# Kernel optimization log

Measured on AMD Instinct MI355X. Metric: run time of the kernel, lower is better.

Reference implementation:

```python
import jax, jax.numpy as jnp
import numpy as np

C = 512
NUM_HEADS = 8
GROUPS = 32
EPS_GN = 1e-5
EPS_ATTN = 1e-6


def setup_inputs() -> dict:
    key = jax.random.key(0)
    ks = jax.random.split(key, 7)
    B, H, W = 8, 64, 64
    x = jax.random.normal(ks[0], (B, C, H, W), dtype=jnp.float32)
    # GroupNorm affine (torch default: weight=1, bias=0)
    norm_gamma = jnp.ones((C,), dtype=jnp.float32)
    norm_beta = jnp.zeros((C,), dtype=jnp.float32)
    # 1x1 conv weights stored as (out, in); torch Conv2d kaiming-ish scale
    qkv_w = jax.random.normal(ks[1], (3 * C, C), dtype=jnp.float32) * (1.0 / np.sqrt(C))
    qkv_b = jax.random.normal(ks[2], (3 * C,), dtype=jnp.float32) * 0.01
    proj_w = jax.random.normal(ks[3], (C, C), dtype=jnp.float32) * (1.0 / np.sqrt(C))
    proj_b = jax.random.normal(ks[4], (C,), dtype=jnp.float32) * 0.01
    return {"x": x, "norm_gamma": norm_gamma, "norm_beta": norm_beta,
            "qkv_w": qkv_w, "qkv_b": qkv_b, "proj_w": proj_w, "proj_b": proj_b}


def _group_norm(x, gamma, beta):
    B, Cc, H, W = x.shape
    xg = x.reshape(B, GROUPS, Cc // GROUPS, H, W)
    mean = xg.mean(axis=(2, 3, 4), keepdims=True)
    var = xg.var(axis=(2, 3, 4), keepdims=True)
    xn = (xg - mean) * jax.lax.rsqrt(var + EPS_GN)
    xn = xn.reshape(B, Cc, H, W)
    return xn * gamma[None, :, None, None] + beta[None, :, None, None]


def reference(x, norm_gamma, norm_beta, qkv_w, qkv_b, proj_w, proj_b):
    B, Cc, H, W = x.shape
    h, d = NUM_HEADS, Cc // NUM_HEADS
    N = H * W
    x_norm = _group_norm(x, norm_gamma, norm_beta)
    # 1x1 conv == channel GEMM
    qkv = jnp.einsum('bchw,oc->bohw', x_norm, qkv_w) + qkv_b[None, :, None, None]
    q, k, v = jnp.split(qkv, 3, axis=1)
    # (B, C, H, W) -> (B, h, N, d)
    def to_heads(t):
        return t.reshape(B, h, d, N).transpose(0, 1, 3, 2)
    q, k, v = to_heads(q), to_heads(k), to_heads(v)
    # phi(x) = elu(x) + 1
    q = jax.nn.elu(q) + 1.0
    k = jax.nn.elu(k) + 1.0
    kv = jnp.einsum('bhnd,bhne->bhde', k, v)          # (B,h,d,d)
    out = jnp.einsum('bhnd,bhde->bhne', q, kv)        # (B,h,N,d)
    denom = jnp.einsum('bhnd,bhd->bhn', q, k.sum(axis=2))
    out = out / (denom[..., None] + EPS_ATTN)
    # (B,h,N,d) -> (B,C,H,W)
    attn = out.transpose(0, 1, 3, 2).reshape(B, Cc, H, W)
    proj = jnp.einsum('bchw,oc->bohw', attn, proj_w) + proj_b[None, :, None, None]
    # dropout is identity at inference
    return x + proj
```

## Files before the change

### kernel.cpp

```cpp
#include <hip/hip_runtime.h>
#include <math.h>

#define BATCH   8
#define CCH     512
#define NHEADS  8
#define HD      64
#define NGROUPS 32
#define CPG     16
#define NSP     4096
#define O1      1536

typedef __attribute__((ext_vector_type(8))) short          short8;
typedef __attribute__((ext_vector_type(8))) unsigned short ushort8;
typedef __attribute__((ext_vector_type(4))) unsigned short ushort4v;
typedef __attribute__((ext_vector_type(4))) float          float4v;

#define GLOAD_LDS16(g, s) __builtin_amdgcn_global_load_lds(                   \
    (const __attribute__((address_space(1))) void*)(g),                       \
    (__attribute__((address_space(3))) void*)(s), 16, 0, 0)

__device__ __forceinline__ float phi_act(float v) {
    return v > 0.f ? v + 1.f : __expf(v);
}
__device__ __forceinline__ unsigned short f2bf(float f) {
    union { float f; unsigned int u; } c; c.f = f;
    unsigned int u = c.u;
    u += 0x7fffu + ((u >> 16) & 1u);
    return (unsigned short)(u >> 16);
}
__device__ __forceinline__ float bf2f(unsigned short s) {
    union { unsigned int u; float f; } c; c.u = ((unsigned int)s) << 16;
    return c.f;
}


__global__ __launch_bounds__(256) void gn_stats(const float* __restrict__ x,
                                                const float* __restrict__ gamma,
                                                const float* __restrict__ beta,
                                                float* __restrict__ ss) {
    const int bg = blockIdx.x;
    const int t  = threadIdx.x;
    const float* base = x + (size_t)bg * (CPG * NSP);
    float s = 0.f, s2 = 0.f;
    #pragma unroll 4
    for (int i = 0; i < 64; ++i) {
        float4 v = *(const float4*)(base + (i * 256 + t) * 4);
        s  += v.x + v.y + v.z + v.w;
        s2 += v.x * v.x + v.y * v.y + v.z * v.z + v.w * v.w;
    }
    __shared__ float r1[256], r2[256];
    r1[t] = s; r2[t] = s2;
    __syncthreads();
    for (int off = 128; off > 0; off >>= 1) {
        if (t < off) { r1[t] += r1[t + off]; r2[t] += r2[t + off]; }
        __syncthreads();
    }
    if (t < CPG) {
        const float inv = 1.f / 65536.f;
        float mean = r1[0] * inv;
        float var  = r2[0] * inv - mean * mean;
        float rstd = rsqrtf(var + 1e-5f);
        int b = bg / NGROUPS, g = bg % NGROUPS;
        int c = g * CPG + t;
        float sc = gamma[c] * rstd;
        float sh = beta[c] - mean * sc;
        ss[(b * CCH + c) * 2]     = sc;
        ss[(b * CCH + c) * 2 + 1] = sh;
    }
}

__global__ __launch_bounds__(256) void conv_w(const float* __restrict__ qw,
                                              const float* __restrict__ pw,
                                              unsigned short* __restrict__ qwb,
                                              unsigned short* __restrict__ pwb,
                                              float* __restrict__ ksum) {
    int i = (blockIdx.x * 256 + threadIdx.x) * 4;
    if (i < O1 * CCH) {
        float4 v = *(const float4*)(qw + i);
        unsigned short o[4] = {f2bf(v.x), f2bf(v.y), f2bf(v.z), f2bf(v.w)};
        *(uint2*)(qwb + i) = *(uint2*)o;
    } else {
        int j = i - O1 * CCH;
        float4 v = *(const float4*)(pw + j);
        unsigned short o[4] = {f2bf(v.x), f2bf(v.y), f2bf(v.z), f2bf(v.w)};
        *(uint2*)(pwb + j) = *(uint2*)o;
    }
    if (blockIdx.x == 0) {
        float4 z = {0.f, 0.f, 0.f, 0.f};
        #pragma unroll
        for (int l = 0; l < 4; ++l)
            *(float4*)(ksum + (l * 256 + threadIdx.x) * 4) = z;
    }
}

__global__ __launch_bounds__(256) void xnT_kernel(const float* __restrict__ x,
                                                  const float* __restrict__ ss,
                                                  unsigned short* __restrict__ xnT) {
    const int n0 = blockIdx.x * 64, c0 = blockIdx.y * 64, b = blockIdx.z;
    const int t = threadIdx.x;
    __shared__ float tile[64][65];
    const float* xb  = x + ((size_t)b * CCH + c0) * NSP + n0;
    const float* ssb = ss + b * CCH * 2;

    const int lr = t / 16, lc = (t % 16) * 4;
    #pragma unroll
    for (int j = 0; j < 4; ++j) {
        int cr = j * 16 + lr;
        float4 v = *(const float4*)(xb + (size_t)cr * NSP + lc);
        float sc = ssb[(c0 + cr) * 2], sh = ssb[(c0 + cr) * 2 + 1];
        tile[cr][lc + 0] = v.x * sc + sh;
        tile[cr][lc + 1] = v.y * sc + sh;
        tile[cr][lc + 2] = v.z * sc + sh;
        tile[cr][lc + 3] = v.w * sc + sh;
    }
    __syncthreads();
    #pragma unroll
    for (int j = 0; j < 2; ++j) {
        int wd = j * 256 + t;
        int n  = wd >> 3;
        int cb = (wd & 7) * 8;
        ushort8 o;
        #pragma unroll
        for (int i = 0; i < 8; ++i) o[i] = f2bf(tile[cb + i][n]);
        *(ushort8*)(xnT + ((size_t)b * NSP + n0 + n) * CCH + c0 + cb) = o;
    }
}

__global__ __launch_bounds__(256) void gemm_q(const unsigned short* __restrict__ A,
                                              const unsigned short* __restrict__ Bt,
                                              const float* __restrict__ bias,
                                              unsigned short* __restrict__ qT) {
    const int n0 = blockIdx.x * 128;
    const int o0 = blockIdx.y * 128;
    const int b  = blockIdx.z;
    const int t  = threadIdx.x;
    const int wv = t >> 6, ln = t & 63;
    const int quad = ln >> 4, lm = ln & 15;
    const int wo = (wv >> 1) * 64, wn = (wv & 1) * 64;

    __shared__ __align__(16) unsigned short As[128 * 64];
    __shared__ __align__(16) unsigned short Bs[128 * 64];

    float4v acc[4][4];
    #pragma unroll
    for (int i = 0; i < 4; ++i)
        #pragma unroll
        for (int j = 0; j < 4; ++j) acc[i][j] = {0.f, 0.f, 0.f, 0.f};

    const unsigned short* aBase = A + (size_t)o0 * CCH;
    const unsigned short* bBase = Bt + ((size_t)b * NSP + n0) * CCH;

    const int srow8 = ln >> 3;
    const int scs   = ((ln & 7) ^ srow8) * 8;
    const int lmp   = (lm & 7);

    for (int k0 = 0; k0 < CCH; k0 += 64) {
        __syncthreads();
        #pragma unroll
        for (int i = 0; i < 4; ++i) {
            int slab = wv + i * 4;
            GLOAD_LDS16(aBase + (size_t)(slab * 8 + srow8) * CCH + k0 + scs,
                        As + slab * 512);
            GLOAD_LDS16(bBase + (size_t)(slab * 8 + srow8) * CCH + k0 + scs,
                        Bs + slab * 512);
        }
        __syncthreads();
        #pragma unroll
        for (int kk = 0; kk < 2; ++kk) {
            const int sc8 = ((kk * 4 + quad) ^ lmp) * 8;
            short8 fw[4], fx[4];
            #pragma unroll
            for (int i = 0; i < 4; ++i)
                fw[i] = *(const short8*)(As + (wo + i * 16 + lm) * 64 + sc8);
            #pragma unroll
            for (int j = 0; j < 4; ++j)
                fx[j] = *(const short8*)(Bs + (wn + j * 16 + lm) * 64 + sc8);
            #pragma unroll
            for (int i = 0; i < 4; ++i)
                #pragma unroll
                for (int j = 0; j < 4; ++j)
                    acc[i][j] = __builtin_amdgcn_mfma_f32_16x16x32_bf16(
                        fw[i], fx[j], acc[i][j], 0, 0, 0);
        }
    }

    #pragma unroll
    for (int i = 0; i < 4; ++i) {
        int ob = o0 + wo + i * 16 + quad * 4;
        float4 b4 = *(const float4*)(bias + ob);
        float bs[4] = {b4.x, b4.y, b4.z, b4.w};
        #pragma unroll
        for (int j = 0; j < 4; ++j) {
            int n = n0 + wn + j * 16 + lm;
            ushort4v pk;
            #pragma unroll
            for (int r = 0; r < 4; ++r)
                pk[r] = f2bf(phi_act(acc[i][j][r] + bs[r]));
            *(ushort4v*)(qT + ((size_t)b * NSP + n) * CCH + ob) = pk;
        }
    }
}

__global__ __launch_bounds__(256) void gemm_kv(const unsigned short* __restrict__ A,
                                               const unsigned short* __restrict__ Bt,
                                               const float* __restrict__ bias,
                                               unsigned short* __restrict__ kb,
                                               unsigned short* __restrict__ vb,
                                               float* __restrict__ ksum) {
    const int n0 = blockIdx.x * 128;
    const int o0 = 512 + blockIdx.y * 128;
    const int b  = blockIdx.z;
    const int t  = threadIdx.x;
    const int wv = t >> 6, ln = t & 63;
    const int quad = ln >> 4, lm = ln & 15;
    const int wo = (wv >> 1) * 64, wn = (wv & 1) * 64;

    __shared__ __align__(16) unsigned short As[128 * 64];
    __shared__ __align__(16) unsigned short Bs[128 * 64];

    float4v acc[4][4];
    #pragma unroll
    for (int i = 0; i < 4; ++i)
        #pragma unroll
        for (int j = 0; j < 4; ++j) acc[i][j] = {0.f, 0.f, 0.f, 0.f};

    const unsigned short* aBase = A + (size_t)o0 * CCH;
    const unsigned short* bBase = Bt + ((size_t)b * NSP + n0) * CCH;

    const int srow8 = ln >> 3;
    const int scs   = ((ln & 7) ^ srow8) * 8;
    const int lmp   = (lm & 7);

    for (int k0 = 0; k0 < CCH; k0 += 64) {
        __syncthreads();
        #pragma unroll
        for (int i = 0; i < 4; ++i) {
            int slab = wv + i * 4;
            GLOAD_LDS16(aBase + (size_t)(slab * 8 + srow8) * CCH + k0 + scs,
                        As + slab * 512);
            GLOAD_LDS16(bBase + (size_t)(slab * 8 + srow8) * CCH + k0 + scs,
                        Bs + slab * 512);
        }
        __syncthreads();
        #pragma unroll
        for (int kk = 0; kk < 2; ++kk) {
            const int sc8 = ((kk * 4 + quad) ^ lmp) * 8;
            short8 fw[4], fx[4];
            #pragma unroll
            for (int i = 0; i < 4; ++i)
                fw[i] = *(const short8*)(As + (wo + i * 16 + lm) * 64 + sc8);
            #pragma unroll
            for (int j = 0; j < 4; ++j)
                fx[j] = *(const short8*)(Bs + (wn + j * 16 + lm) * 64 + sc8);
            #pragma unroll
            for (int i = 0; i < 4; ++i)
                #pragma unroll
                for (int j = 0; j < 4; ++j)
                    acc[i][j] = __builtin_amdgcn_mfma_f32_16x16x32_bf16(
                        fx[j], fw[i], acc[i][j], 0, 0, 0);
        }
    }

    const bool isk = (o0 < 1024);
    unsigned short* dst = isk ? kb : vb;
    const int cb0 = o0 - (isk ? 512 : 1024);
    #pragma unroll
    for (int i = 0; i < 4; ++i) {
        int o = o0 + wo + i * 16 + lm;
        int c = cb0 + wo + i * 16 + lm;
        float bs = bias[o];
        float ksp = 0.f;
        #pragma unroll
        for (int j = 0; j < 4; ++j) {
            int n = n0 + wn + j * 16 + quad * 4;
            ushort4v pk;
            #pragma unroll
            for (int r = 0; r < 4; ++r) {
                float v = acc[i][j][r] + bs;
                if (isk) { v = phi_act(v); ksp += v; }
                pk[r] = f2bf(v);
            }
            *(ushort4v*)(dst + ((size_t)b * CCH + c) * NSP + n) = pk;
        }
        if (isk) {
            ksp += __shfl_xor(ksp, 16);
            ksp += __shfl_xor(ksp, 32);
            if (quad == 0) atomicAdd(ksum + b * CCH + c, ksp);
        }
    }
}

__global__ __launch_bounds__(256) void kv_mfma(const unsigned short* __restrict__ kb,
                                               const unsigned short* __restrict__ vb,
                                               float* __restrict__ kvp) {
    const int chunk = blockIdx.x, bh = blockIdx.y;
    const int b = bh >> 3, h = bh & 7;
    const int t = threadIdx.x;
    const int wv = t >> 6, ln = t & 63;
    const int quad = ln >> 4, lm = ln & 15;
    const int wd = (wv >> 1) * 32, we = (wv & 1) * 32;

    __shared__ __align__(16) unsigned short kt[2 * 64 * 32];
    __shared__ __align__(16) unsigned short vt[2 * 64 * 32];

    float4v acc[2][2];
    #pragma unroll
    for (int i = 0; i < 2; ++i)
        #pragma unroll
        for (int j = 0; j < 2; ++j) acc[i][j] = {0.f, 0.f, 0.f, 0.f};

    const unsigned short* kbase = kb + ((size_t)b * CCH + h * 64) * NSP + chunk * 1024;
    const unsigned short* vbase = vb + ((size_t)b * CCH + h * 64) * NSP + chunk * 1024;
    const int srow = ln >> 2;
    const int scs  = ((ln & 3) ^ ((ln >> 3) & 3)) * 8;
    const int sc8  = (quad ^ ((lm >> 1) & 3)) * 8;

    for (int it = 0; it < 16; ++it) {
        int noff = it * 64;
        __syncthreads();
        GLOAD_LDS16(kbase + (size_t)(wv * 16 + srow) * NSP + noff + scs,      kt + wv * 512);
        GLOAD_LDS16(kbase + (size_t)(wv * 16 + srow) * NSP + noff + 32 + scs, kt + 2048 + wv * 512);
        GLOAD_LDS16(vbase + (size_t)(wv * 16 + srow) * NSP + noff + scs,      vt + wv * 512);
        GLOAD_LDS16(vbase + (size_t)(wv * 16 + srow) * NSP + noff + 32 + scs, vt + 2048 + wv * 512);
        __syncthreads();
        #pragma unroll
        for (int kk = 0; kk < 2; ++kk) {
            short8 a0 = *(const short8*)(kt + kk * 2048 + (wd + lm) * 32 + sc8);
            short8 a1 = *(const short8*)(kt + kk * 2048 + (wd + 16 + lm) * 32 + sc8);
            short8 b0 = *(const short8*)(vt + kk * 2048 + (we + lm) * 32 + sc8);
            short8 b1 = *(const short8*)(vt + kk * 2048 + (we + 16 + lm) * 32 + sc8);
            acc[0][0] = __builtin_amdgcn_mfma_f32_16x16x32_bf16(a0, b0, acc[0][0], 0, 0, 0);
            acc[0][1] = __builtin_amdgcn_mfma_f32_16x16x32_bf16(a0, b1, acc[0][1], 0, 0, 0);
            acc[1][0] = __builtin_amdgcn_mfma_f32_16x16x32_bf16(a1, b0, acc[1][0], 0, 0, 0);
            acc[1][1] = __builtin_amdgcn_mfma_f32_16x16x32_bf16(a1, b1, acc[1][1], 0, 0, 0);
        }
    }
    #pragma unroll
    for (int i = 0; i < 2; ++i)
        #pragma unroll
        for (int j = 0; j < 2; ++j) {
            int e = we + j * 16 + lm;
            int d = wd + i * 16 + quad * 4;
            float4 r = {acc[i][j][0], acc[i][j][1], acc[i][j][2], acc[i][j][3]};
            *(float4*)(kvp + ((size_t)(chunk * 64 + bh) * 64 + e) * 64 + d) = r;
        }
}

__global__ __launch_bounds__(256) void kv_reduce(const float* __restrict__ kvp,
                                                 unsigned short* __restrict__ kvTb) {
    int idx4 = (blockIdx.x * 256 + threadIdx.x) * 4;
    float4 s = {0.f, 0.f, 0.f, 0.f};
    #pragma unroll
    for (int p = 0; p < 4; ++p) {
        float4 v = *(const float4*)(kvp + (size_t)p * (64 * 64 * 64) + idx4);
        s.x += v.x; s.y += v.y; s.z += v.z; s.w += v.w;
    }
    ushort4v o = {f2bf(s.x), f2bf(s.y), f2bf(s.z), f2bf(s.w)};
    *(ushort4v*)(kvTb + idx4) = o;
}

__global__ __launch_bounds__(256) void attn_mfma(const unsigned short* __restrict__ qT,
                                                 const unsigned short* __restrict__ kvTb,
                                                 const float* __restrict__ ksum,
                                                 unsigned short* __restrict__ attnT) {
    const int n0 = blockIdx.x * 256;
    const int bh = blockIdx.y;
    const int b = bh >> 3, h = bh & 7;
    const int t = threadIdx.x;
    const int wv = t >> 6, ln = t & 63;
    const int quad = ln >> 4, lm = ln & 15;
    const int nb = n0 + wv * 64;

    __shared__ __align__(16) unsigned short kvs[64 * 72];
    __shared__ float kss[64];

    #pragma unroll
    for (int l = 0; l < 2; ++l) {
        int ch = l * 256 + t;
        int e = ch >> 3, c8 = ch & 7;
        *(ushort8*)(kvs + e * 72 + c8 * 8) =
            *(const ushort8*)(kvTb + (size_t)bh * 4096 + ch * 8);
    }
    if (t < 64) kss[t] = ksum[b * CCH + h * 64 + t];
    __syncthreads();

    short8 bq[4][2];
    #pragma unroll
    for (int j = 0; j < 4; ++j)
        #pragma unroll
        for (int kk = 0; kk < 2; ++kk) {
            int n = nb + j * 16 + lm;
            bq[j][kk] = *(const short8*)(qT + ((size_t)b * NSP + n) * CCH +
                                         h * 64 + kk * 32 + quad * 8);
        }
    short8 ak[4][2];
    #pragma unroll
    for (int i = 0; i < 4; ++i)
        #pragma unroll
        for (int kk = 0; kk < 2; ++kk)
            ak[i][kk] = *(const short8*)(kvs + (i * 16 + lm) * 72 + kk * 32 + quad * 8);

    float4v acc[4][4];
    #pragma unroll
    for (int i = 0; i < 4; ++i)
        #pragma unroll
        for (int j = 0; j < 4; ++j) acc[i][j] = {0.f, 0.f, 0.f, 0.f};
    #pragma unroll
    for (int kk = 0; kk < 2; ++kk)
        #pragma unroll
        for (int i = 0; i < 4; ++i)
            #pragma unroll
            for (int j = 0; j < 4; ++j)
                acc[i][j] = __builtin_amdgcn_mfma_f32_16x16x32_bf16(
                    ak[i][kk], bq[j][kk], acc[i][j], 0, 0, 0);

    float rden[4];
    #pragma unroll
    for (int j = 0; j < 4; ++j) {
        float dp = 0.f;
        #pragma unroll
        for (int kk = 0; kk < 2; ++kk)
            #pragma unroll
            for (int l = 0; l < 8; ++l)
                dp += bf2f((unsigned short)bq[j][kk][l]) * kss[kk * 32 + quad * 8 + l];
        dp += __shfl_xor(dp, 16);
        dp += __shfl_xor(dp, 32);
        rden[j] = 1.f / (dp + 1e-6f);
    }

    #pragma unroll
    for (int i = 0; i < 4; ++i) {
        int e = i * 16 + quad * 4;
        #pragma unroll
        for (int j = 0; j < 4; ++j) {
            int n = nb + j * 16 + lm;
            ushort4v pk;
            #pragma unroll
            for (int r = 0; r < 4; ++r)
                pk[r] = f2bf(acc[i][j][r] * rden[j]);
            *(ushort4v*)(attnT + ((size_t)b * NSP + n) * CCH + h * 64 + e) = pk;
        }
    }
}

__global__ __launch_bounds__(256) void gemm_proj(const unsigned short* __restrict__ A,
                                                 const unsigned short* __restrict__ Bt,
                                                 const float* __restrict__ bias,
                                                 const float* __restrict__ resid,
                                                 float* __restrict__ outF) {
    const int n0 = blockIdx.x * 128;
    const int o0 = blockIdx.y * 128;
    const int b  = blockIdx.z;
    const int t  = threadIdx.x;
    const int wv = t >> 6, ln = t & 63;
    const int quad = ln >> 4, lm = ln & 15;
    const int wo = (wv >> 1) * 64, wn = (wv & 1) * 64;

    __shared__ __align__(16) unsigned short As[128 * 64];
    __shared__ __align__(16) unsigned short Bs[128 * 64];

    float4v acc[4][4];
    #pragma unroll
    for (int i = 0; i < 4; ++i)
        #pragma unroll
        for (int j = 0; j < 4; ++j) acc[i][j] = {0.f, 0.f, 0.f, 0.f};

    const unsigned short* aBase = A + (size_t)o0 * CCH;
    const unsigned short* bBase = Bt + ((size_t)b * NSP + n0) * CCH;

    const int srow8 = ln >> 3;
    const int scs   = ((ln & 7) ^ srow8) * 8;
    const int lmp   = (lm & 7);

    for (int k0 = 0; k0 < CCH; k0 += 64) {
        __syncthreads();
        #pragma unroll
        for (int i = 0; i < 4; ++i) {
            int slab = wv + i * 4;
            GLOAD_LDS16(aBase + (size_t)(slab * 8 + srow8) * CCH + k0 + scs,
                        As + slab * 512);
            GLOAD_LDS16(bBase + (size_t)(slab * 8 + srow8) * CCH + k0 + scs,
                        Bs + slab * 512);
        }
        __syncthreads();
        #pragma unroll
        for (int kk = 0; kk < 2; ++kk) {
            const int sc8 = ((kk * 4 + quad) ^ lmp) * 8;
            short8 fw[4], fx[4];
            #pragma unroll
            for (int i = 0; i < 4; ++i)
                fw[i] = *(const short8*)(As + (wo + i * 16 + lm) * 64 + sc8);
            #pragma unroll
            for (int j = 0; j < 4; ++j)
                fx[j] = *(const short8*)(Bs + (wn + j * 16 + lm) * 64 + sc8);
            #pragma unroll
            for (int i = 0; i < 4; ++i)
                #pragma unroll
                for (int j = 0; j < 4; ++j)
                    acc[i][j] = __builtin_amdgcn_mfma_f32_16x16x32_bf16(
                        fx[j], fw[i], acc[i][j], 0, 0, 0);
        }
    }

    #pragma unroll
    for (int i = 0; i < 4; ++i) {
        int o = o0 + wo + i * 16 + lm;
        float bs = bias[o];
        #pragma unroll
        for (int j = 0; j < 4; ++j) {
            int n = n0 + wn + j * 16 + quad * 4;
            size_t off = ((size_t)b * CCH + o) * NSP + n;
            float4 rv = *(const float4*)(resid + off);
            float4 w = {acc[i][j][0] + bs + rv.x, acc[i][j][1] + bs + rv.y,
                        acc[i][j][2] + bs + rv.z, acc[i][j][3] + bs + rv.w};
            *(float4*)(outF + off) = w;
        }
    }
}

extern "C" void kernel_launch(void* const* d_in, const int* in_sizes, int n_in,
                              void* d_out, int out_size, void* d_ws, size_t ws_size,
                              hipStream_t stream) {
    const float* x      = (const float*)d_in[0];
    const float* gamma  = (const float*)d_in[1];
    const float* beta   = (const float*)d_in[2];
    const float* qkv_w  = (const float*)d_in[3];
    const float* qkv_b  = (const float*)d_in[4];
    const float* proj_w = (const float*)d_in[5];
    const float* proj_b = (const float*)d_in[6];
    float* out = (float*)d_out;

    float* ws   = (float*)d_ws;
    float* ss   = ws;
    float* ksum = ss + 8192;
    float* kvp  = ksum + 4096;
    unsigned short* xnT   = (unsigned short*)(kvp + 4 * 64 * 64 * 64);
    unsigned short* qT    = xnT + (size_t)BATCH * NSP * CCH;
    unsigned short* kb    = qT  + (size_t)BATCH * NSP * CCH;
    unsigned short* vb    = kb  + (size_t)BATCH * NSP * CCH;
    unsigned short* attnT = vb  + (size_t)BATCH * NSP * CCH;
    unsigned short* kvTb  = attnT + (size_t)BATCH * NSP * CCH;
    unsigned short* wqb   = kvTb + (size_t)64 * 64 * 64;
    unsigned short* wpb   = wqb + (size_t)O1 * CCH;

    gn_stats<<<BATCH * NGROUPS, 256, 0, stream>>>(x, gamma, beta, ss);
    conv_w<<<(O1 * CCH + CCH * CCH) / 4 / 256, 256, 0, stream>>>(qkv_w, proj_w, wqb, wpb, ksum);
    xnT_kernel<<<dim3(NSP / 64, CCH / 64, BATCH), 256, 0, stream>>>(x, ss, xnT);

    gemm_q <<<dim3(NSP / 128, 4, BATCH), 256, 0, stream>>>(wqb, xnT, qkv_b, qT);
    gemm_kv<<<dim3(NSP / 128, 8, BATCH), 256, 0, stream>>>(wqb, xnT, qkv_b, kb, vb, ksum);

    kv_mfma<<<dim3(4, 64), 256, 0, stream>>>(kb, vb, kvp);
    kv_reduce<<<256, 256, 0, stream>>>(kvp, kvTb);
    attn_mfma<<<dim3(NSP / 256, 64), 256, 0, stream>>>(qT, kvTb, ksum, attnT);

    gemm_proj<<<dim3(NSP / 128, CCH / 128, BATCH), 256, 0, stream>>>(
        wpb, attnT, proj_b, x, out);
}
```

Measured before the change: 295.3 us.

## Fuse per-head K/V projection with partial KV outer-product in gemm_kv

gemm_kv now computes the K and V rows of one head for a 128-position tile and stages the bf16 results in shared memory instead of writing kb/vb to global memory. It then immediately computes the partial k^T v product for that tile and writes one fp32 partial per tile. The separate kv_mfma kernel and the kb/vb buffers go away, along with a launch and the low-parallelism KV pass. In exchange there are 32 partial KV matrices instead of 4, which enlarges the kvp buffer and the kv_reduce read traffic, and an extra LDS round-trip and barrier are added in the GEMM epilogue.

```diff
diff --git a/kernel.cpp b/kernel.cpp
--- a/kernel.cpp
+++ b/kernel.cpp
@@ -204,19 +204,17 @@
 __global__ __launch_bounds__(256) void gemm_kv(const unsigned short* __restrict__ A,
                                                const unsigned short* __restrict__ Bt,
                                                const float* __restrict__ bias,
-                                               unsigned short* __restrict__ kb,
-                                               unsigned short* __restrict__ vb,
-                                               float* __restrict__ ksum) {
+                                               float* __restrict__ ksum,
+                                               float* __restrict__ kvp) {
     const int n0 = blockIdx.x * 128;
-    const int o0 = 512 + blockIdx.y * 128;
+    const int h  = blockIdx.y;
     const int b  = blockIdx.z;
     const int t  = threadIdx.x;
     const int wv = t >> 6, ln = t & 63;
     const int quad = ln >> 4, lm = ln & 15;
     const int wo = (wv >> 1) * 64, wn = (wv & 1) * 64;
 
-    __shared__ __align__(16) unsigned short As[128 * 64];
-    __shared__ __align__(16) unsigned short Bs[128 * 64];
+    __shared__ __align__(16) unsigned short sh[2 * 128 * 64];
 
     float4v acc[4][4];
     #pragma unroll
@@ -224,7 +222,8 @@
         #pragma unroll
         for (int j = 0; j < 4; ++j) acc[i][j] = {0.f, 0.f, 0.f, 0.f};
 
-    const unsigned short* aBase = A + (size_t)o0 * CCH;
+    const unsigned short* aK = A + (size_t)(512 + h * 64) * CCH;
+    const unsigned short* aV = A + (size_t)(1024 + h * 64) * CCH;
     const unsigned short* bBase = Bt + ((size_t)b * NSP + n0) * CCH;
 
     const int srow8 = ln >> 3;
@@ -236,10 +235,12 @@
         #pragma unroll
         for (int i = 0; i < 4; ++i) {
             int slab = wv + i * 4;
-            GLOAD_LDS16(aBase + (size_t)(slab * 8 + srow8) * CCH + k0 + scs,
-                        As + slab * 512);
+            const unsigned short* ab = (slab < 8)
+                ? aK + (size_t)(slab * 8 + srow8) * CCH
+                : aV + (size_t)((slab - 8) * 8 + srow8) * CCH;
+            GLOAD_LDS16(ab + k0 + scs, sh + slab * 512);
             GLOAD_LDS16(bBase + (size_t)(slab * 8 + srow8) * CCH + k0 + scs,
-                        Bs + slab * 512);
+                        sh + 8192 + slab * 512);
         }
         __syncthreads();
         #pragma unroll
@@ -248,10 +249,10 @@
             short8 fw[4], fx[4];
             #pragma unroll
             for (int i = 0; i < 4; ++i)
-                fw[i] = *(const short8*)(As + (wo + i * 16 + lm) * 64 + sc8);
+                fw[i] = *(const short8*)(sh + (wo + i * 16 + lm) * 64 + sc8);
             #pragma unroll
             for (int j = 0; j < 4; ++j)
-                fx[j] = *(const short8*)(Bs + (wn + j * 16 + lm) * 64 + sc8);
+                fx[j] = *(const short8*)(sh + 8192 + (wn + j * 16 + lm) * 64 + sc8);
             #pragma unroll
             for (int i = 0; i < 4; ++i)
                 #pragma unroll
@@ -261,87 +262,80 @@
         }
     }
 
-    const bool isk = (o0 < 1024);
-    unsigned short* dst = isk ? kb : vb;
-    const int cb0 = o0 - (isk ? 512 : 1024);
+    __syncthreads();
+    const bool isk = (wv < 2);
+    const float* bptr = bias + (isk ? 512 : 1024) + h * 64;
+    float ksp[4] = {0.f, 0.f, 0.f, 0.f};
     #pragma unroll
     for (int i = 0; i < 4; ++i) {
-        int o = o0 + wo + i * 16 + lm;
-        int c = cb0 + wo + i * 16 + lm;
-        float bs = bias[o];
-        float ksp = 0.f;
+        float bs = bptr[i * 16 + lm];
+        int row = wo + i * 16 + lm;
         #pragma unroll
         for (int j = 0; j < 4; ++j) {
-            int n = n0 + wn + j * 16 + quad * 4;
+            int n = wn + j * 16 + quad * 4;
             ushort4v pk;
             #pragma unroll
             for (int r = 0; r < 4; ++r) {
                 float v = acc[i][j][r] + bs;
-                if (isk) { v = phi_act(v); ksp += v; }
+                if (isk) { v = phi_act(v); ksp[i] += v; }
                 pk[r] = f2bf(v);
             }
-            *(ushort4v*)(dst + ((size_t)b * CCH + c) * NSP + n) = pk;
-        }
-        if (isk) {
-            ksp += __shfl_xor(ksp, 16);
-            ksp += __shfl_xor(ksp, 32);
-            if (quad == 0) atomicAdd(ksum + b * CCH + c, ksp);
-        }
-    }
-}
-
-__global__ __launch_bounds__(256) void kv_mfma(const unsigned short* __restrict__ kb,
-                                               const unsigned short* __restrict__ vb,
-                                               float* __restrict__ kvp) {
-    const int chunk = blockIdx.x, bh = blockIdx.y;
-    const int b = bh >> 3, h = bh & 7;
-    const int t = threadIdx.x;
-    const int wv = t >> 6, ln = t & 63;
-    const int quad = ln >> 4, lm = ln & 15;
+            int idx = row * 128 + ((((n >> 3) ^ (row & 15)) << 3) | (n & 7));
+            *(ushort4v*)(sh + idx) = pk;
+        }
+    }
+    if (isk) {
+        #pragma unroll
+        for (int i = 0; i < 4; ++i) {
+            float s = ksp[i];
+            s += __shfl_xor(s, 16);
+            s += __shfl_xor(s, 32);
+            if (quad == 0)
+                atomicAdd(ksum + b * CCH + h * 64 + i * 16 + lm, s);
+        }
+    }
+    __syncthreads();
+
     const int wd = (wv >> 1) * 32, we = (wv & 1) * 32;
-
-    __shared__ __align__(16) unsigned short kt[2 * 64 * 32];
-    __shared__ __align__(16) unsigned short vt[2 * 64 * 32];
-
-    float4v acc[2][2];
+    float4v acc2[2][2];
     #pragma unroll
     for (int i = 0; i < 2; ++i)
         #pragma unroll
-        for (int j = 0; j < 2; ++j) acc[i][j] = {0.f, 0.f, 0.f, 0.f};
-
-    const unsigned short* kbase = kb + ((size_t)b * CCH + h * 64) * NSP + chunk * 1024;
-    const unsigned short* vbase = vb + ((size_t)b * CCH + h * 64) * NSP + chunk * 1024;
-    const int srow = ln >> 2;
-    const int scs  = ((ln & 3) ^ ((ln >> 3) & 3)) * 8;
-    const int sc8  = (quad ^ ((lm >> 1) & 3)) * 8;
-
-    for (int it = 0; it < 16; ++it) {
-        int noff = it * 64;
-        __syncthreads();
-        GLOAD_LDS16(kbase + (size_t)(wv * 16 + srow) * NSP + noff + scs,      kt + wv * 512);
-        GLOAD_LDS16(kbase + (size_t)(wv * 16 + srow) * NSP + noff + 32 + scs, kt + 2048 + wv * 512);
-        GLOAD_LDS16(vbase + (size_t)(wv * 16 + srow) * NSP + noff + scs,      vt + wv * 512);
-        GLOAD_LDS16(vbase + (size_t)(wv * 16 + srow) * NSP + noff + 32 + scs, vt + 2048 + wv * 512);
-        __syncthreads();
-        #pragma unroll
-        for (int kk = 0; kk < 2; ++kk) {
-            short8 a0 = *(const short8*)(kt + kk * 2048 + (wd + lm) * 32 + sc8);
-            short8 a1 = *(const short8*)(kt + kk * 2048 + (wd + 16 + lm) * 32 + sc8);
-            short8 b0 = *(const short8*)(vt + kk * 2048 + (we + lm) * 32 + sc8);
-            short8 b1 = *(const short8*)(vt + kk * 2048 + (we + 16 + lm) * 32 + sc8);
-            acc[0][0] = __builtin_amdgcn_mfma_f32_16x16x32_bf16(a0, b0, acc[0][0], 0, 0, 0);
-            acc[0][1] = __builtin_amdgcn_mfma_f32_16x16x32_bf16(a0, b1, acc[0][1], 0, 0, 0);
-            acc[1][0] = __builtin_amdgcn_mfma_f32_16x16x32_bf16(a1, b0, acc[1][0], 0, 0, 0);
-            acc[1][1] = __builtin_amdgcn_mfma_f32_16x16x32_bf16(a1, b1, acc[1][1], 0, 0, 0);
-        }
-    }
-    #pragma unroll
-    for (int i = 0; i < 2; ++i)
-        #pragma unroll
-        for (int j = 0; j < 2; ++j) {
-            int e = we + j * 16 + lm;
-            int d = wd + i * 16 + quad * 4;
-            float4 r = {acc[i][j][0], acc[i][j][1], acc[i][j][2], acc[i][j][3]};
+        for (int j = 0; j < 2; ++j) acc2[i][j] = {0.f, 0.f, 0.f, 0.f};
+
+    #pragma unroll
+    for (int ks = 0; ks < 4; ++ks) {
+        short8 ka[2], vbf[2];
+        #pragma unroll
+        for (int i2 = 0; i2 < 2; ++i2) {
+            int row = wd + i2 * 16 + lm;
+            ka[i2] = *(const short8*)(sh + row * 128 +
+                                      (((ks * 4 + quad) ^ (row & 15)) << 3));
+        }
+        #pragma unroll
+        for (int j2 = 0; j2 < 2; ++j2) {
+            int row = 64 + we + j2 * 16 + lm;
+            vbf[j2] = *(const short8*)(sh + row * 128 +
+                                       (((ks * 4 + quad) ^ (row & 15)) << 3));
+        }
+        #pragma unroll
+        for (int i2 = 0; i2 < 2; ++i2)
+            #pragma unroll
+            for (int j2 = 0; j2 < 2; ++j2)
+                acc2[i2][j2] = __builtin_amdgcn_mfma_f32_16x16x32_bf16(
+                    ka[i2], vbf[j2], acc2[i2][j2], 0, 0, 0);
+    }
+
+    const int chunk = blockIdx.x;
+    const int bh = b * 8 + h;
+    #pragma unroll
+    for (int i2 = 0; i2 < 2; ++i2)
+        #pragma unroll
+        for (int j2 = 0; j2 < 2; ++j2) {
+            int e = we + j2 * 16 + lm;
+            int d = wd + i2 * 16 + quad * 4;
+            float4 r = {acc2[i2][j2][0], acc2[i2][j2][1],
+                        acc2[i2][j2][2], acc2[i2][j2][3]};
             *(float4*)(kvp + ((size_t)(chunk * 64 + bh) * 64 + e) * 64 + d) = r;
         }
 }
@@ -351,7 +345,7 @@
     int idx4 = (blockIdx.x * 256 + threadIdx.x) * 4;
     float4 s = {0.f, 0.f, 0.f, 0.f};
     #pragma unroll
-    for (int p = 0; p < 4; ++p) {
+    for (int p = 0; p < 32; ++p) {
         float4 v = *(const float4*)(kvp + (size_t)p * (64 * 64 * 64) + idx4);
         s.x += v.x; s.y += v.y; s.z += v.z; s.w += v.w;
     }
@@ -534,11 +528,9 @@
     float* ss   = ws;
     float* ksum = ss + 8192;
     float* kvp  = ksum + 4096;
-    unsigned short* xnT   = (unsigned short*)(kvp + 4 * 64 * 64 * 64);
+    unsigned short* xnT   = (unsigned short*)(kvp + (size_t)32 * 64 * 64 * 64);
     unsigned short* qT    = xnT + (size_t)BATCH * NSP * CCH;
-    unsigned short* kb    = qT  + (size_t)BATCH * NSP * CCH;
-    unsigned short* vb    = kb  + (size_t)BATCH * NSP * CCH;
-    unsigned short* attnT = vb  + (size_t)BATCH * NSP * CCH;
+    unsigned short* attnT = qT  + (size_t)BATCH * NSP * CCH;
     unsigned short* kvTb  = attnT + (size_t)BATCH * NSP * CCH;
     unsigned short* wqb   = kvTb + (size_t)64 * 64 * 64;
     unsigned short* wpb   = wqb + (size_t)O1 * CCH;
@@ -548,9 +540,8 @@
     xnT_kernel<<<dim3(NSP / 64, CCH / 64, BATCH), 256, 0, stream>>>(x, ss, xnT);
 
     gemm_q <<<dim3(NSP / 128, 4, BATCH), 256, 0, stream>>>(wqb, xnT, qkv_b, qT);
-    gemm_kv<<<dim3(NSP / 128, 8, BATCH), 256, 0, stream>>>(wqb, xnT, qkv_b, kb, vb, ksum);
-
-    kv_mfma<<<dim3(4, 64), 256, 0, stream>>>(kb, vb, kvp);
+    gemm_kv<<<dim3(NSP / 128, NHEADS, BATCH), 256, 0, stream>>>(wqb, xnT, qkv_b, ksum, kvp);
+
     kv_reduce<<<256, 256, 0, stream>>>(kvp, kvTb);
     attn_mfma<<<dim3(NSP / 256, 64), 256, 0, stream>>>(qT, kvTb, ksum, attnT);
 
```

Result: faster. 286.2 us (-3.1%).
